# Performance work log

Measured on AMD Instinct MI355X. Metric: run time of the kernel, lower is better.

## Reference

```python
import jax, jax.numpy as jnp
import numpy as np

NEG = -1000000000.0

def setup_inputs() -> dict:
    key = jax.random.key(0)
    k1, k2, k3, k4 = jax.random.split(key, 4)
    B, Sq, Sk, D = 8, 2048, 2048, 1024
    query = jax.random.normal(k1, (B, Sq, D), dtype=jnp.float32)
    memories = jax.random.normal(k2, (B, Sk, D), dtype=jnp.float32)
    mask = jax.random.randint(k3, (B, Sq, Sk), 0, 2).astype(jnp.int32)
    W = jax.random.normal(k4, (D, D), dtype=jnp.float32) * (1.0 / np.sqrt(D))
    b = jnp.zeros((D,), dtype=jnp.float32)
    return {"query": query, "memories": memories, "mask": mask, "W": W, "b": b}

def reference(query, memories, mask, W, b):
    # linear projection: nn.Linear applies x @ W^T + b
    q = jnp.einsum('bsd,od->bso', query, W) + b
    add_mask = (1.0 - mask.astype(q.dtype)) * NEG
    # [B,Sq,Sk] attention logits
    attn_logits = jnp.einsum('bqd,bkd->bqk', q, memories) + add_mask
    attn_weights = jax.nn.softmax(attn_logits, axis=-1)
    attn_outputs = jnp.einsum('bqk,bkd->bqd', attn_weights, memories)
    return attn_outputs
```

## Files before the change

### kernel.cpp

```cpp
#include <hip/hip_runtime.h>


typedef __attribute__((ext_vector_type(8))) _Float16 f16x8;
typedef __attribute__((ext_vector_type(4))) float f32x4;
typedef unsigned short u16;
typedef unsigned int u32;

#define B_ 8
#define SQL 2048
#define SKL 2048
#define DD 1024
#define NEGC -1000000000.0f

static __device__ __forceinline__ u16 f2h(float x) {
  _Float16 h = (_Float16)x;
  return __builtin_bit_cast(u16, h);
}
static __device__ __forceinline__ float h2f(u16 v) {
  return (float)__builtin_bit_cast(_Float16, v);
}
static __device__ __forceinline__ void gload16(const void* g, void* l) {
  __builtin_amdgcn_global_load_lds((const __attribute__((address_space(1))) u32*)g,
                                   (__attribute__((address_space(3))) u32*)l, 16, 0, 0);
}

__global__ __launch_bounds__(256) void prep_k(const float* __restrict__ query,
                                              u16* __restrict__ q16,
                                              const float* __restrict__ Wm,
                                              u16* __restrict__ wh, u16* __restrict__ wl) {
  if (blockIdx.x < 2048) {
    long n = (long)B_ * SQL * DD;
    long i = ((long)blockIdx.x * 256 + threadIdx.x) * 8;
    long stride = 2048L * 256 * 8;
    for (; i < n; i += stride) {
      float4 v0 = *(const float4*)(query + i);
      float4 v1 = *(const float4*)(query + i + 4);
      ushort4 o0 = make_ushort4(f2h(v0.x), f2h(v0.y), f2h(v0.z), f2h(v0.w));
      ushort4 o1 = make_ushort4(f2h(v1.x), f2h(v1.y), f2h(v1.z), f2h(v1.w));
      *(ushort4*)(q16 + i) = o0;
      *(ushort4*)(q16 + i + 4) = o1;
    }
  } else {
    long i = ((long)(blockIdx.x - 2048) * 256 + threadIdx.x) * 8;
    float4 v0 = *(const float4*)(Wm + i);
    float4 v1 = *(const float4*)(Wm + i + 4);
    u16 h0 = f2h(v0.x), h1 = f2h(v0.y), h2 = f2h(v0.z), h3 = f2h(v0.w);
    u16 h4 = f2h(v1.x), h5 = f2h(v1.y), h6 = f2h(v1.z), h7 = f2h(v1.w);
    *(ushort4*)(wh + i) = make_ushort4(h0, h1, h2, h3);
    *(ushort4*)(wh + i + 4) = make_ushort4(h4, h5, h6, h7);
    *(ushort4*)(wl + i) = make_ushort4(f2h(v0.x - h2f(h0)), f2h(v0.y - h2f(h1)),
                                       f2h(v0.z - h2f(h2)), f2h(v0.w - h2f(h3)));
    *(ushort4*)(wl + i + 4) = make_ushort4(f2h(v1.x - h2f(h4)), f2h(v1.y - h2f(h5)),
                                           f2h(v1.z - h2f(h6)), f2h(v1.w - h2f(h7)));
  }
}

__global__ __launch_bounds__(256, 2) void proj_split_k(
    const u16* __restrict__ Ah, const u16* __restrict__ Bh, const u16* __restrict__ Bl,
    const float* __restrict__ bias, u16* __restrict__ C0,
    const float* __restrict__ mem, u16* __restrict__ memh, u16* __restrict__ memT) {
  __shared__ u16 lA[256 * 64];
  __shared__ u16 lB[128 * 128];

  if (blockIdx.x < 512) {
    const int N = DD, K = DD;
    int id = blockIdx.x;
    int j = (id & 7) * 64 + (id >> 3);
    const int TX = N >> 7;
    const int by = j / TX, bx = j % TX;
    const int tid = threadIdx.x;
    const int l = tid & 63, w = tid >> 6;
    const int wr = w >> 1, wc = w & 1;
    const long am0 = (long)by * 256;
    const long bn0 = (long)bx * 128;

    f32x4 acc[8][4];
#pragma unroll
    for (int i = 0; i < 8; ++i)
#pragma unroll
      for (int j2 = 0; j2 < 4; ++j2) {
        f32x4 z = {0.f, 0.f, 0.f, 0.f};
        acc[i][j2] = z;
      }
    const int lrow = l & 15, lch = l >> 4;

    for (int k0 = 0; k0 < K; k0 += 64) {
      __syncthreads();
#pragma unroll
      for (int i = 0; i < 8; ++i) {
        int row = i * 32 + (tid >> 3);
        int cc = (tid & 7) ^ (row & 7);
        gload16(Ah + (am0 + row) * K + k0 + cc * 8, &lA[row * 64 + (tid & 7) * 8]);
      }
#pragma unroll
      for (int i = 0; i < 8; ++i) {
        int row = i * 16 + (tid >> 4);
        int s = tid & 15;
        int cc = s ^ (row & 15);
        const u16* src = (cc < 8) ? (Bh + (bn0 + row) * K + k0 + cc * 8)
                                  : (Bl + (bn0 + row) * K + k0 + (cc - 8) * 8);
        gload16(src, &lB[row * 128 + s * 8]);
      }
      __syncthreads();

#pragma unroll
      for (int kk = 0; kk < 2; ++kk) {
        f16x8 ah[8], bh[4], bl_[4];
#pragma unroll
        for (int f = 0; f < 8; ++f) {
          int ra = wr * 128 + f * 16 + lrow;
          int c = kk * 4 + lch;
          ah[f] = *(const f16x8*)&lA[ra * 64 + (c ^ (ra & 7)) * 8];
        }
#pragma unroll
        for (int f = 0; f < 4; ++f) {
          int rb = wc * 64 + f * 16 + lrow;
          int c = kk * 4 + lch;
          bh[f] = *(const f16x8*)&lB[rb * 128 + (c ^ (rb & 15)) * 8];
          bl_[f] = *(const f16x8*)&lB[rb * 128 + ((8 + c) ^ (rb & 15)) * 8];
        }
#pragma unroll
        for (int mf = 0; mf < 8; ++mf)
#pragma unroll
          for (int nf = 0; nf < 4; ++nf) {
            acc[mf][nf] = __builtin_amdgcn_mfma_f32_16x16x32_f16(ah[mf], bh[nf], acc[mf][nf], 0, 0, 0);
            acc[mf][nf] = __builtin_amdgcn_mfma_f32_16x16x32_f16(ah[mf], bl_[nf], acc[mf][nf], 0, 0, 0);
          }
      }
    }
#pragma unroll
    for (int mf = 0; mf < 8; ++mf)
#pragma unroll
      for (int nf = 0; nf < 4; ++nf)
#pragma unroll
        for (int r = 0; r < 4; ++r) {
          long row = am0 + wr * 128 + mf * 16 + (l >> 4) * 4 + r;
          long col = bn0 + wc * 64 + nf * 16 + (l & 15);
          C0[row * N + col] = f2h(acc[mf][nf][r] + bias[col]);
        }
  } else {
    u16(*t)[65] = (u16(*)[65])lA;
    int id2 = blockIdx.x - 512;
    int bx = id2 & 15, by = (id2 >> 4) & 31, bz = id2 >> 9;
    long bo = (long)bz * SKL * DD;
    int r0 = by * 64, c0 = bx * 64;
    int tr = threadIdx.x / 16, tc4 = (threadIdx.x % 16) * 4;
#pragma unroll
    for (int i = 0; i < 4; ++i) {
      int r = tr + i * 16;
      long idx = bo + (long)(r0 + r) * DD + c0 + tc4;
      float4 v = *(const float4*)(mem + idx);
      u16 h0 = f2h(v.x), h1 = f2h(v.y), h2 = f2h(v.z), h3 = f2h(v.w);
      *(ushort4*)(memh + idx) = make_ushort4(h0, h1, h2, h3);
      t[r][tc4 + 0] = h0; t[r][tc4 + 1] = h1; t[r][tc4 + 2] = h2; t[r][tc4 + 3] = h3;
    }
    __syncthreads();
#pragma unroll
    for (int i = 0; i < 4; ++i) {
      int c = tr + i * 16;
      ushort4 v = make_ushort4(t[tc4 + 0][c], t[tc4 + 1][c], t[tc4 + 2][c], t[tc4 + 3][c]);
      *(ushort4*)(memT + bo + (long)(c0 + c) * SKL + r0 + tc4) = v;
    }
  }
}

template <int OUTMODE>
__global__ __launch_bounds__(256, 2) void gemm1_f16(
    const u16* __restrict__ Ah, const u16* __restrict__ Bh,
    void* __restrict__ C0,
    int N, int K, int TPB, long batchA, long batchB, long batchC) {
  __shared__ u16 lA[256 * 64];
  __shared__ u16 lB[128 * 64];

  const int nwg = gridDim.x;
  int id = blockIdx.x;
  int j = (id & 7) * (nwg >> 3) + (id >> 3);
  const int TX = N >> 7;
  const int bz = j / TPB;
  const int r0_ = j % TPB;
  const int by = r0_ / TX, bx = r0_ % TX;

  const u16* pAh = Ah + (long)bz * batchA;
  const u16* pBh = Bh + (long)bz * batchB;

  const int tid = threadIdx.x;
  const int l = tid & 63, w = tid >> 6;
  const int wr = w >> 1, wc = w & 1;
  const long am0 = (long)by * 256;
  const long bn0 = (long)bx * 128;

  f32x4 acc[8][4];
#pragma unroll
  for (int i = 0; i < 8; ++i)
#pragma unroll
    for (int j2 = 0; j2 < 4; ++j2) {
      f32x4 z = {0.f, 0.f, 0.f, 0.f};
      acc[i][j2] = z;
    }
  const int lrow = l & 15, lch = l >> 4;

  for (int k0 = 0; k0 < K; k0 += 64) {
    __syncthreads();
#pragma unroll
    for (int i = 0; i < 8; ++i) {
      int row = i * 32 + (tid >> 3);
      int cc = (tid & 7) ^ (row & 7);
      gload16(pAh + (am0 + row) * K + k0 + cc * 8, &lA[row * 64 + (tid & 7) * 8]);
    }
#pragma unroll
    for (int i = 0; i < 4; ++i) {
      int row = i * 32 + (tid >> 3);
      int cc = (tid & 7) ^ (row & 7);
      gload16(pBh + (bn0 + row) * K + k0 + cc * 8, &lB[row * 64 + (tid & 7) * 8]);
    }
    __syncthreads();

#pragma unroll
    for (int kk = 0; kk < 2; ++kk) {
      f16x8 ah[8], bh[4];
#pragma unroll
      for (int f = 0; f < 8; ++f) {
        int ra = wr * 128 + f * 16 + lrow;
        int c = kk * 4 + lch;
        ah[f] = *(const f16x8*)&lA[ra * 64 + (c ^ (ra & 7)) * 8];
      }
#pragma unroll
      for (int f = 0; f < 4; ++f) {
        int rb = wc * 64 + f * 16 + lrow;
        int c = kk * 4 + lch;
        bh[f] = *(const f16x8*)&lB[rb * 64 + (c ^ (rb & 7)) * 8];
      }
#pragma unroll
      for (int mf = 0; mf < 8; ++mf)
#pragma unroll
        for (int nf = 0; nf < 4; ++nf)
          acc[mf][nf] = __builtin_amdgcn_mfma_f32_16x16x32_f16(ah[mf], bh[nf], acc[mf][nf], 0, 0, 0);
    }
  }

#pragma unroll
  for (int mf = 0; mf < 8; ++mf)
#pragma unroll
    for (int nf = 0; nf < 4; ++nf)
#pragma unroll
      for (int r = 0; r < 4; ++r) {
        long row = am0 + wr * 128 + mf * 16 + (l >> 4) * 4 + r;
        long col = bn0 + wc * 64 + nf * 16 + (l & 15);
        long idx = (long)bz * batchC + row * N + col;
        if (OUTMODE == 0) ((float*)C0)[idx] = acc[mf][nf][r];
        else              ((u16*)C0)[idx] = f2h(acc[mf][nf][r]);
      }
}

__global__ __launch_bounds__(256) void softmax16_k(const float* __restrict__ S,
                                                   const int* __restrict__ M,
                                                   u16* __restrict__ P) {
  long row = (long)blockIdx.x * 4 + (threadIdx.x >> 6);
  const float* s = S + row * SKL;
  const int* m = M + row * SKL;
  u16* p = P + row * SKL;
  const int lane = threadIdx.x & 63;
  float x[32];
#pragma unroll
  for (int j = 0; j < 8; ++j) {
    float4 v = *(const float4*)(s + lane * 4 + j * 256);
    int4 q = *(const int4*)(m + lane * 4 + j * 256);
    x[j * 4 + 0] = q.x ? v.x : v.x + NEGC;
    x[j * 4 + 1] = q.y ? v.y : v.y + NEGC;
    x[j * 4 + 2] = q.z ? v.z : v.z + NEGC;
    x[j * 4 + 3] = q.w ? v.w : v.w + NEGC;
  }
  float mx = x[0];
#pragma unroll
  for (int j = 1; j < 32; ++j) mx = fmaxf(mx, x[j]);
#pragma unroll
  for (int o = 32; o >= 1; o >>= 1) mx = fmaxf(mx, __shfl_xor(mx, o, 64));
  float sum = 0.f;
#pragma unroll
  for (int j = 0; j < 32; ++j) { x[j] = __expf(x[j] - mx); sum += x[j]; }
#pragma unroll
  for (int o = 32; o >= 1; o >>= 1) sum += __shfl_xor(sum, o, 64);
  float inv = 1.f / sum;
#pragma unroll
  for (int j = 0; j < 8; ++j) {
    ushort4 o4 = make_ushort4(f2h(x[j * 4 + 0] * inv), f2h(x[j * 4 + 1] * inv),
                              f2h(x[j * 4 + 2] * inv), f2h(x[j * 4 + 3] * inv));
    *(ushort4*)(p + lane * 4 + j * 256) = o4;
  }
}

extern "C" void kernel_launch(void* const* d_in, const int* in_sizes, int n_in,
                              void* d_out, int out_size, void* d_ws, size_t ws_size,
                              hipStream_t stream) {
  const float* query = (const float*)d_in[0];
  const float* mem = (const float*)d_in[1];
  const int* mask = (const int*)d_in[2];
  const float* Wm = (const float*)d_in[3];
  const float* bias = (const float*)d_in[4];
  float* out = (float*)d_out;

  const long nQ = (long)B_ * SQL * DD;
  const long nW = (long)DD * DD;
  const long nS = (long)B_ * SQL * SKL;

  char* ws = (char*)d_ws;
  u16* q16 = (u16*)ws; ws += nQ * 2;
  u16* memh = (u16*)ws; ws += nQ * 2;
  u16* memT = (u16*)ws; ws += nQ * 2;
  u16* q1 = (u16*)ws; ws += nQ * 2;
  u16* wh = (u16*)ws; ws += nW * 2;
  u16* wl = (u16*)ws; ws += nW * 2;
  float* S = (float*)ws; ws += nS * 4;
  u16* P = q16;

  prep_k<<<2048 + 512, 256, 0, stream>>>(query, q16, Wm, wh, wl);
  proj_split_k<<<512 + 4096, 256, 0, stream>>>(q16, wh, wl, bias, q1, mem, memh, memT);
  gemm1_f16<0><<<1024, 256, 0, stream>>>(
      q1, memh, S, SKL, DD, 128,
      (long)SQL * DD, (long)SKL * DD, (long)SQL * SKL);
  softmax16_k<<<(B_ * SQL) / 4, 256, 0, stream>>>(S, mask, P);
  gemm1_f16<0><<<512, 256, 0, stream>>>(
      P, memT, out, DD, SKL, 64,
      (long)SQL * SKL, (long)DD * SKL, (long)SQL * DD);
}
```

Measured before the change: 315.2 us.

## Use 256x256 double-buffered GEMM with interleaved prefetch and 8 waves

Replaces the single-buffered 256x128 GEMM with a 512-thread, 256x256 tile kernel. It double-buffers the A and B tiles in LDS and issues the next k-step's global-to-LDS loads in four quarters, interleaved with the MFMA phases. It also raises wave priority around the MFMA blocks. The aim is to hide load latency behind compute and raise arithmetic intensity per loaded byte. The cost is 128KB of LDS per block, which limits occupancy to one block per CU, and the larger tiles halve the grid sizes.

```diff
diff --git a/kernel.cpp b/kernel.cpp
--- a/kernel.cpp
+++ b/kernel.cpp
@@ -165,29 +165,31 @@
 }
 
 template <int OUTMODE>
-__global__ __launch_bounds__(256, 2) void gemm1_f16(
+__global__ __launch_bounds__(512, 2) void gemm8_f16(
     const u16* __restrict__ Ah, const u16* __restrict__ Bh,
     void* __restrict__ C0,
     int N, int K, int TPB, long batchA, long batchB, long batchC) {
-  __shared__ u16 lA[256 * 64];
-  __shared__ u16 lB[128 * 64];
+  __shared__ u16 lA[2][256 * 64];
+  __shared__ u16 lB[2][256 * 64];
 
   const int nwg = gridDim.x;
   int id = blockIdx.x;
   int j = (id & 7) * (nwg >> 3) + (id >> 3);
-  const int TX = N >> 7;
+  const int TX = N >> 8;
   const int bz = j / TPB;
   const int r0_ = j % TPB;
   const int by = r0_ / TX, bx = r0_ % TX;
 
-  const u16* pAh = Ah + (long)bz * batchA;
-  const u16* pBh = Bh + (long)bz * batchB;
+  const u16* pA = Ah + (long)bz * batchA;
+  const u16* pB = Bh + (long)bz * batchB;
 
   const int tid = threadIdx.x;
   const int l = tid & 63, w = tid >> 6;
-  const int wr = w >> 1, wc = w & 1;
+  const int wr = w >> 2, wc = w & 3;
   const long am0 = (long)by * 256;
-  const long bn0 = (long)bx * 128;
+  const long bn0 = (long)bx * 256;
+  const int lrow = l & 15, lch = l >> 4;
+  const int srow = tid >> 3, schunk = tid & 7;
 
   f32x4 acc[8][4];
 #pragma unroll
@@ -197,44 +199,76 @@
       f32x4 z = {0.f, 0.f, 0.f, 0.f};
       acc[i][j2] = z;
     }
-  const int lrow = l & 15, lch = l >> 4;
-
-  for (int k0 = 0; k0 < K; k0 += 64) {
-    __syncthreads();
-#pragma unroll
-    for (int i = 0; i < 8; ++i) {
-      int row = i * 32 + (tid >> 3);
-      int cc = (tid & 7) ^ (row & 7);
-      gload16(pAh + (am0 + row) * K + k0 + cc * 8, &lA[row * 64 + (tid & 7) * 8]);
-    }
-#pragma unroll
-    for (int i = 0; i < 4; ++i) {
-      int row = i * 32 + (tid >> 3);
-      int cc = (tid & 7) ^ (row & 7);
-      gload16(pBh + (bn0 + row) * K + k0 + cc * 8, &lB[row * 64 + (tid & 7) * 8]);
-    }
-    __syncthreads();
-
-#pragma unroll
-    for (int kk = 0; kk < 2; ++kk) {
-      f16x8 ah[8], bh[4];
-#pragma unroll
-      for (int f = 0; f < 8; ++f) {
-        int ra = wr * 128 + f * 16 + lrow;
-        int c = kk * 4 + lch;
-        ah[f] = *(const f16x8*)&lA[ra * 64 + (c ^ (ra & 7)) * 8];
-      }
-#pragma unroll
-      for (int f = 0; f < 4; ++f) {
-        int rb = wc * 64 + f * 16 + lrow;
-        int c = kk * 4 + lch;
-        bh[f] = *(const f16x8*)&lB[rb * 64 + (c ^ (rb & 7)) * 8];
-      }
-#pragma unroll
-      for (int mf = 0; mf < 8; ++mf)
-#pragma unroll
-        for (int nf = 0; nf < 4; ++nf)
-          acc[mf][nf] = __builtin_amdgcn_mfma_f32_16x16x32_f16(ah[mf], bh[nf], acc[mf][nf], 0, 0, 0);
+
+  auto STAGE_HALF = [&](int buf, int isB, int half, int k0) {
+    const u16* p = isB ? pB : pA;
+    long b0 = isB ? bn0 : am0;
+    u16* dst = isB ? &lB[buf][0] : &lA[buf][0];
+#pragma unroll
+    for (int i = 0; i < 2; ++i) {
+      int row = half * 128 + i * 64 + srow;
+      int cc = schunk ^ (row & 7);
+      gload16(p + (b0 + row) * K + k0 + cc * 8, dst + row * 64 + schunk * 8);
+    }
+  };
+
+  STAGE_HALF(0, 0, 0, 0); STAGE_HALF(0, 0, 1, 0);
+  STAGE_HALF(0, 1, 0, 0); STAGE_HALF(0, 1, 1, 0);
+  asm volatile("s_waitcnt vmcnt(0)" ::: "memory");
+  __builtin_amdgcn_sched_barrier(0);
+  __builtin_amdgcn_s_barrier();
+
+  const int KITER = K >> 6;
+  for (int t = 0; t < KITER; ++t) {
+    const int c = t & 1;
+    const int k1 = (t + 1) << 6;
+    const bool more = (t + 1 < KITER);
+
+    f16x8 bfr[4][2];
+#pragma unroll
+    for (int nf = 0; nf < 4; ++nf)
+#pragma unroll
+      for (int kk = 0; kk < 2; ++kk) {
+        int rb = wc * 64 + nf * 16 + lrow;
+        int cch = kk * 4 + lch;
+        bfr[nf][kk] = *(const f16x8*)&lB[c][rb * 64 + (cch ^ (rb & 7)) * 8];
+      }
+
+#pragma unroll
+    for (int p = 0; p < 4; ++p) {
+      f16x8 afr[2][2];
+#pragma unroll
+      for (int mi = 0; mi < 2; ++mi)
+#pragma unroll
+        for (int kk = 0; kk < 2; ++kk) {
+          int ra = wr * 128 + (2 * p + mi) * 16 + lrow;
+          int cch = kk * 4 + lch;
+          afr[mi][kk] = *(const f16x8*)&lA[c][ra * 64 + (cch ^ (ra & 7)) * 8];
+        }
+      if (more) {
+        if (p == 0)      STAGE_HALF(c ^ 1, 0, 0, k1);
+        else if (p == 1) STAGE_HALF(c ^ 1, 0, 1, k1);
+        else if (p == 2) STAGE_HALF(c ^ 1, 1, 0, k1);
+        else             STAGE_HALF(c ^ 1, 1, 1, k1);
+      }
+      __builtin_amdgcn_s_barrier();
+      __builtin_amdgcn_s_setprio(1);
+#pragma unroll
+      for (int kk = 0; kk < 2; ++kk)
+#pragma unroll
+        for (int mi = 0; mi < 2; ++mi)
+#pragma unroll
+          for (int nf = 0; nf < 4; ++nf)
+            acc[2 * p + mi][nf] = __builtin_amdgcn_mfma_f32_16x16x32_f16(
+                afr[mi][kk], bfr[nf][kk], acc[2 * p + mi][nf], 0, 0, 0);
+      __builtin_amdgcn_s_setprio(0);
+      __builtin_amdgcn_s_barrier();
+    }
+
+    if (more) {
+      asm volatile("s_waitcnt vmcnt(0)" ::: "memory");
+      __builtin_amdgcn_sched_barrier(0);
+      __builtin_amdgcn_s_barrier();
     }
   }
 
@@ -315,11 +349,11 @@
 
   prep_k<<<2048 + 512, 256, 0, stream>>>(query, q16, Wm, wh, wl);
   proj_split_k<<<512 + 4096, 256, 0, stream>>>(q16, wh, wl, bias, q1, mem, memh, memT);
-  gemm1_f16<0><<<1024, 256, 0, stream>>>(
-      q1, memh, S, SKL, DD, 128,
+  gemm8_f16<0><<<512, 512, 0, stream>>>(
+      q1, memh, S, SKL, DD, 64,
       (long)SQL * DD, (long)SKL * DD, (long)SQL * SKL);
   softmax16_k<<<(B_ * SQL) / 4, 256, 0, stream>>>(S, mask, P);
-  gemm1_f16<0><<<512, 256, 0, stream>>>(
-      P, memT, out, DD, SKL, 64,
+  gemm8_f16<0><<<256, 512, 0, stream>>>(
+      P, memT, out, DD, SKL, 32,
       (long)SQL * SKL, (long)DD * SKL, (long)SQL * DD);
 }
```

Measured after the change: 339.4 us. 7.7% more time.
